# Kernel tuning notes

Measured on AMD Instinct MI355X. Metric: run time of the kernel, lower is better.

The kernel has to match this reference:

```python
import jax, jax.numpy as jnp
import numpy as np

K = 3  # kernel_size


def _build_grid(offset, H, W):
    """Vectorized version of the original double for-loop grid build.

    Original: for x in range(W), y in range(H):
        anchor = ([x, y] - [W-1, H-1]/2) / ([W-1, H-1]/2)
        fgrid[:, K*y:K*y+K, K*x:K*x+K, :] = offset[:, :, x, y].view(B, K, K, 2) + anchor
    Note offset is indexed [:, :, x, y] (x over range(W) on the H axis) -- requires H == W.
    """
    B = offset.shape[0]
    assert H == W, "original indexing offset[:, :, x, y] assumes square maps"
    o = offset.reshape(B, K, K, 2, H, W)          # [B, j, i, c, x-axis, y-axis]
    # -> [B, y, j, x, i, c] so rows are K*y+j, cols are K*x+i
    o = jnp.transpose(o, (0, 5, 1, 4, 2, 3))
    half_w = (W - 1) / 2.0
    half_h = (H - 1) / 2.0
    ax = ((jnp.arange(W, dtype=offset.dtype) - half_w) / half_w)  # anchor x-coord, indexed by x
    ay = ((jnp.arange(H, dtype=offset.dtype) - half_h) / half_h)  # anchor y-coord, indexed by y
    anch = jnp.stack(jnp.broadcast_arrays(ax[None, :], ay[:, None]), axis=-1)  # [H(y), W(x), 2]
    grid = o + anch[None, :, None, :, None, :]
    return grid.reshape(B, H * K, W * K, 2)


def _grid_sample_bilinear(img, grid):
    """F.grid_sample(img, grid, mode='bilinear', padding_mode='zeros', align_corners=False)."""
    B, C, H, W = img.shape
    gx, gy = grid[..., 0], grid[..., 1]          # [B, Ho, Wo]
    ix = ((gx + 1.0) * W - 1.0) * 0.5            # unnormalize, align_corners=False
    iy = ((gy + 1.0) * H - 1.0) * 0.5
    ix0 = jnp.floor(ix)
    iy0 = jnp.floor(iy)
    wx1 = ix - ix0
    wy1 = iy - iy0
    flat = img.reshape(B, C, H * W)

    def gather(xi, yi):
        valid = ((xi >= 0) & (xi <= W - 1) & (yi >= 0) & (yi <= H - 1))
        xc = jnp.clip(xi, 0, W - 1).astype(jnp.int32)
        yc = jnp.clip(yi, 0, H - 1).astype(jnp.int32)
        lin = (yc * W + xc).reshape(B, -1)       # [B, Ho*Wo]
        g = jax.vmap(lambda f, l: f[:, l])(flat, lin)  # [B, C, Ho*Wo]
        g = g.reshape(B, C, *xi.shape[1:])
        return g * valid[:, None].astype(img.dtype)

    out = (gather(ix0, iy0) * ((1 - wx1) * (1 - wy1))[:, None]
           + gather(ix0 + 1, iy0) * (wx1 * (1 - wy1))[:, None]
           + gather(ix0, iy0 + 1) * ((1 - wx1) * wy1)[:, None]
           + gather(ix0 + 1, iy0 + 1) * (wx1 * wy1)[:, None])
    return out


def setup_inputs() -> dict:
    key = jax.random.key(0)
    k1, k2, k3 = jax.random.split(key, 3)
    B, C, H, W = 32, 128, 56, 56
    OUTC = 256
    feature = jax.random.normal(k1, (B, C, H, W), dtype=jnp.float32)
    offset = jax.random.normal(k2, (B, 2 * K * K, H, W), dtype=jnp.float32) * 0.1
    conv_weight = jax.random.normal(k3, (OUTC, C, K, K), dtype=jnp.float32) * 0.05
    return {"feature": feature, "offset": offset, "conv_weight": conv_weight}


def reference(feature, offset, conv_weight):
    B, C, H, W = feature.shape
    grid = _build_grid(offset, H, W)                      # [B, H*K, W*K, 2]
    deformed = _grid_sample_bilinear(feature, grid)       # [B, C, H*K, W*K]
    out = jax.lax.conv_general_dilated(
        deformed, conv_weight, window_strides=(K, K), padding="VALID",
        dimension_numbers=("NCHW", "OIHW", "NCHW"))      # [B, OUTC, H, W]
    return out
```

## Files before the change

kernel.cpp:

```cpp
#include <hip/hip_runtime.h>
#include <hip/hip_bf16.h>
#include <stdint.h>

#define KTAPS 9
#define C_IN 128
#define C_OUT 256
#define HW 56
#define PLANE 3136
#define BATCH 32
#define NPX (BATCH * PLANE)
#define KTOT 1152
#define NBLK64 (NPX / 64)
#define BPER (NBLK64 / 8)
#define VBLK_STRIDE (KTAPS * 16384)

typedef __attribute__((ext_vector_type(8))) _Float16 f16x8;
typedef __attribute__((ext_vector_type(2))) _Float16 f16x2;
typedef __attribute__((ext_vector_type(4))) float f32x4;
typedef __attribute__((ext_vector_type(4))) unsigned int u32x4;

static __device__ __forceinline__ uint16_t f2h(float f) {
    _Float16 h = (_Float16)f;
    uint16_t u;
    __builtin_memcpy(&u, &h, 2);
    return u;
}

__global__ void k_feat_nhwc(const float* __restrict__ f, unsigned short* __restrict__ fws) {
    __shared__ float tile[C_IN * 57];
    int blk = blockIdx.x;
    int b = blk / HW, y = blk % HW;
    const float* src = f + (size_t)b * C_IN * PLANE + y * HW;
    for (int i = threadIdx.x; i < C_IN * HW; i += 256) {
        int c = i / HW, x = i % HW;
        tile[c * 57 + x] = src[(size_t)c * PLANE + x];
    }
    __syncthreads();
    unsigned short* dst = fws + (size_t)blk * HW * C_IN;
    for (int j = threadIdx.x; j < HW * C_IN; j += 256) {
        int x = j >> 7, c = j & 127;
        dst[j] = f2h(tile[c * 57 + x]);
    }
}

__global__ void k_weight(const float* __restrict__ w, unsigned short* __restrict__ W3) {
    int idx = blockIdx.x * 256 + threadIdx.x;
    if (idx >= C_OUT * KTOT) return;
    int e = idx & 7;
    int lane = (idx >> 3) & 63;
    int mtg = (idx >> 9) & 15;
    int ks = (idx >> 13) & 3;
    int t = idx >> 15;
    int oc = mtg * 16 + (lane & 15);
    int ic = ks * 32 + (lane >> 4) * 8 + e;
    int j = t / 3, i = t % 3;
    W3[idx] = f2h(w[((oc * C_IN + ic) * 3 + j) * 3 + i]);
}

__global__ void k_coords(const float* __restrict__ off, float* __restrict__ sxy) {
    __shared__ float tile[HW * 57];
    int blk = blockIdx.x;
    int b = blk / 18, tc = blk % 18;
    const float* src = off + (size_t)blk * PLANE;
    for (int i = threadIdx.x; i < PLANE; i += 256) {
        int xx = i / HW, yy = i % HW;
        tile[xx * 57 + yy] = src[i];
    }
    __syncthreads();
    float* dst = sxy + (size_t)tc * NPX + (size_t)b * PLANE;
    bool isx = (tc & 1) == 0;
    for (int p = threadIdx.x; p < PLANE; p += 256) {
        int y = p / HW, x = p % HW;
        float v = tile[x * 57 + y];
        float a = isx ? ((float)x - 27.5f) * (1.0f / 27.5f)
                      : ((float)y - 27.5f) * (1.0f / 27.5f);
        dst[p] = (v + a + 1.0f) * 28.0f - 0.5f;
    }
}

__global__ __launch_bounds__(256, 8) void k_sample(const unsigned short* __restrict__ fws,
                                                   const float* __restrict__ sxy,
                                                   unsigned char* __restrict__ V4) {
    __shared__ float cs[18][64];
    const int tid = threadIdx.x;
    const int wave = tid >> 6, lane = tid & 63;
    const int lb = (blockIdx.x & 7) * BPER + (blockIdx.x >> 3);
    const int gpx0 = lb * 64;
    for (int i = tid; i < 18 * 64; i += 256) {
        int tc = i >> 6, pp = i & 63;
        cs[tc][pp] = sxy[(size_t)tc * NPX + gpx0 + pp];
    }
    __syncthreads();

    const unsigned char* fimg =
        (const unsigned char*)(fws + (size_t)(gpx0 / PLANE) * (PLANE * C_IN));
    unsigned char* vblk = V4 + (size_t)lb * VBLK_STRIDE;
    const int q = lane >> 2, c = lane & 3;
    const int cx = c & 1, cy = c >> 1;
    const int pl = wave * 16 + q;
    const int lane4 = lane * 4;

    uint32_t d[4][4];
    f16x2 wv[4][4];

#pragma unroll
    for (int t = 0; t < KTAPS; t++) {
        float ixv = cs[2 * t][pl], iyv = cs[2 * t + 1][pl];
        float fx0 = floorf(ixv), fy0 = floorf(iyv);
        float wx1 = ixv - fx0, wy1 = iyv - fy0;
        int ix0 = (int)fx0, iy0 = (int)fy0;
        int xi = ix0 + cx, yi = iy0 + cy;
        float wf = (cx ? wx1 : 1.0f - wx1) * (cy ? wy1 : 1.0f - wy1);
        if ((unsigned)xi >= HW || (unsigned)yi >= HW) wf = 0.0f;
        int xc = min(max(xi, 0), HW - 1), yc = min(max(yi, 0), HW - 1);
        int offv = (yc * HW + xc) << 8;
        _Float16 hw_ = (_Float16)wf;
        uint16_t hu;
        __builtin_memcpy(&hu, &hw_, 2);
        int wpk = (int)((uint32_t)hu | ((uint32_t)hu << 16));

        auto ISS = [&](int qq, int slot) {
#pragma unroll
            for (int cc = 0; cc < 4; cc++) {
                int so_ = __builtin_amdgcn_readlane(offv, qq * 4 + cc);
                int wp_ = __builtin_amdgcn_readlane(wpk, qq * 4 + cc);
                __builtin_memcpy(&wv[slot][cc], &wp_, 4);
                d[slot][cc] = *(const uint32_t*)(fimg + so_ + lane4);
            }
        };
        auto FIN = [&](int qq, int slot) {
            f16x2 a0, a1, a2, a3;
            __builtin_memcpy(&a0, &d[slot][0], 4);
            __builtin_memcpy(&a1, &d[slot][1], 4);
            __builtin_memcpy(&a2, &d[slot][2], 4);
            __builtin_memcpy(&a3, &d[slot][3], 4);
            f16x2 v = a0 * wv[slot][0] + a1 * wv[slot][1] + a2 * wv[slot][2] + a3 * wv[slot][3];
            uint32_t u;
            __builtin_memcpy(&u, &v, 4);
            *(uint32_t*)(vblk + (size_t)t * 16384 + (wave * 16 + qq) * 256 + lane4) = u;
        };
        ISS(0, 0); ISS(1, 1); ISS(2, 2); ISS(3, 3);
#pragma unroll
        for (int qq = 0; qq < 16; qq++) {
            FIN(qq, qq & 3);
            if (qq < 12) ISS(qq + 4, (qq + 4) & 3);
        }
    }
}

__global__ __launch_bounds__(256, 3) void k_gemm(const unsigned short* __restrict__ W3,
                                                 const unsigned char* __restrict__ V4,
                                                 float* __restrict__ out) {
    __shared__ __align__(16) unsigned char Vt[2][16384];
    const int tid = threadIdx.x;
    const int wave = tid >> 6, lane = tid & 63;
    const int l16 = lane & 15, grp = lane >> 4;
    const int lb = (blockIdx.x & 7) * BPER + (blockIdx.x >> 3);
    const int gpx0 = lb * 64;
    const unsigned char* vblk = V4 + (size_t)lb * VBLK_STRIDE;

    f32x4 acc[4][4];
#pragma unroll
    for (int m = 0; m < 4; m++)
#pragma unroll
        for (int n = 0; n < 4; n++) acc[m][n] = (f32x4)0.0f;

    f16x8 A[2][4];
    u32x4 sv[4];

    auto SLOAD = [&](int t) {
#pragma unroll
        for (int j = 0; j < 4; j++)
            sv[j] = *(const u32x4*)(vblk + (size_t)t * 16384 + wave * 4096 + j * 1024 + lane * 16);
    };
    auto SWRITE = [&](int buf) {
#pragma unroll
        for (int j = 0; j < 4; j++) {
            int px = wave * 16 + j * 4 + (lane >> 4);
            int c16 = lane & 15;
            *(u32x4*)(&Vt[buf][px * 256 + ((c16 ^ (px & 7)) << 4)]) = sv[j];
        }
    };
    auto loadA = [&](int slot, int t, int ks) {
        const unsigned short* wb = W3 + (size_t)((t * 4 + ks) * 16 + wave * 4) * 512 + lane * 8;
#pragma unroll
        for (int mt = 0; mt < 4; mt++)
            A[slot][mt] = *(const f16x8*)(wb + mt * 512);
    };
    auto gemm_ks = [&](int ks, int buf, int slot) {
        f16x8 bv[4];
#pragma unroll
        for (int nt = 0; nt < 4; nt++) {
            int px = nt * 16 + l16;
            int g16 = ks * 4 + grp;
            bv[nt] = *(const f16x8*)(&Vt[buf][px * 256 + ((g16 ^ (px & 7)) << 4)]);
        }
#pragma unroll
        for (int mt = 0; mt < 4; mt++)
#pragma unroll
            for (int nt = 0; nt < 4; nt++)
                acc[mt][nt] = __builtin_amdgcn_mfma_f32_16x16x32_f16(A[slot][mt], bv[nt], acc[mt][nt], 0, 0, 0);
    };

    SLOAD(0);
    SWRITE(0);
    loadA(0, 0, 0);
    __syncthreads();

#pragma unroll
    for (int t = 0; t < KTAPS; t++) {
        const int buf = t & 1;
        const bool more = (t < KTAPS - 1);
        if (more) SLOAD(t + 1);
        loadA(1, t, 1);
        gemm_ks(0, buf, 0);
        loadA(0, t, 2);
        gemm_ks(1, buf, 1);
        loadA(1, t, 3);
        gemm_ks(2, buf, 0);
        if (more) loadA(0, t + 1, 0);
        gemm_ks(3, buf, 1);
        if (more) {
            __builtin_amdgcn_sched_barrier(0);
            SWRITE(buf ^ 1);
            __syncthreads();
        }
    }

    int bb = gpx0 / PLANE, rr0 = gpx0 - bb * PLANE;
    float* obase = out + (size_t)bb * C_OUT * PLANE + rr0 + l16;
#pragma unroll
    for (int nt = 0; nt < 4; nt++) {
        float* ob = obase + nt * 16;
#pragma unroll
        for (int mt = 0; mt < 4; mt++) {
#pragma unroll
            for (int r = 0; r < 4; r++) {
                int oc = wave * 64 + mt * 16 + grp * 4 + r;
                ob[(size_t)oc * PLANE] = acc[mt][nt][r];
            }
        }
    }
}

__global__ __launch_bounds__(256, 2) void k_fused(const unsigned short* __restrict__ fws,
                                                  const unsigned short* __restrict__ W3,
                                                  const float* __restrict__ sxy,
                                                  float* __restrict__ out) {
    __shared__ float cs[18][64];
    const int tid = threadIdx.x;
    const int wave = tid >> 6, lane = tid & 63;
    const int l16 = lane & 15, grp = lane >> 4;
    const int lbid = (blockIdx.x & 7) * (NBLK64 / 8) + (blockIdx.x >> 3);
    const int px0 = lbid * 64;
    const unsigned short* fb = fws + (size_t)(px0 / PLANE) * (PLANE * C_IN) + grp * 8;
    for (int i = tid; i < 18 * 64; i += 256) {
        int tc = i >> 6, pp = i & 63;
        cs[tc][pp] = sxy[(size_t)tc * NPX + px0 + pp];
    }
    __syncthreads();
    const int p = wave * 16 + l16;
    f32x4 acc[16];
#pragma unroll
    for (int m = 0; m < 16; m++) acc[m] = (f32x4)0.0f;
    f16x8 cv[4][4];
    float swc[4], swn[4];
    const unsigned short *c00, *c10, *c01, *c11;
    auto calc_tap = [&](int t, float* sw) {
        float ixv = cs[2 * t][p], iyv = cs[2 * t + 1][p];
        float fx0 = floorf(ixv), fy0 = floorf(iyv);
        float wx1 = ixv - fx0, wy1 = iyv - fy0;
        float wx0 = 1.0f - wx1, wy0 = 1.0f - wy1;
        int ix0 = (int)fx0, iy0 = (int)fy0, ix1 = ix0 + 1, iy1 = iy0 + 1;
        float vx0 = ((unsigned)ix0 < HW) ? 1.0f : 0.0f;
        float vx1 = ((unsigned)ix1 < HW) ? 1.0f : 0.0f;
        float vy0 = ((unsigned)iy0 < HW) ? 1.0f : 0.0f;
        float vy1 = ((unsigned)iy1 < HW) ? 1.0f : 0.0f;
        int xc0 = min(max(ix0, 0), HW - 1), xc1 = min(max(ix1, 0), HW - 1);
        int yc0 = min(max(iy0, 0), HW - 1), yc1 = min(max(iy1, 0), HW - 1);
        const unsigned short* r0 = fb + (size_t)(yc0 * HW) * C_IN;
        const unsigned short* r1 = fb + (size_t)(yc1 * HW) * C_IN;
        c00 = r0 + xc0 * C_IN; c10 = r0 + xc1 * C_IN;
        c01 = r1 + xc0 * C_IN; c11 = r1 + xc1 * C_IN;
        sw[0] = wx0 * wy0 * vx0 * vy0; sw[1] = wx1 * wy0 * vx1 * vy0;
        sw[2] = wx0 * wy1 * vx0 * vy1; sw[3] = wx1 * wy1 * vx1 * vy1;
    };
    auto sample_ks = [&](int ks) {
        cv[0][ks] = *(const f16x8*)(c00 + ks * 32);
        cv[1][ks] = *(const f16x8*)(c10 + ks * 32);
        cv[2][ks] = *(const f16x8*)(c01 + ks * 32);
        cv[3][ks] = *(const f16x8*)(c11 + ks * 32);
    };
    calc_tap(0, swc);
#pragma unroll
    for (int ks = 0; ks < 4; ks++) sample_ks(ks);
#pragma unroll
    for (int t = 0; t < KTAPS; t++) {
        const bool more = (t < KTAPS - 1);
        if (more) calc_tap(t + 1, swn);
#pragma unroll
        for (int ks = 0; ks < 4; ks++) {
            f16x8 v = cv[0][ks] * (f16x8)(_Float16)swc[0]
                    + cv[1][ks] * (f16x8)(_Float16)swc[1]
                    + cv[2][ks] * (f16x8)(_Float16)swc[2]
                    + cv[3][ks] * (f16x8)(_Float16)swc[3];
            const unsigned short* wb = W3 + (size_t)(t * 4 + ks) * 8192 + lane * 8;
            f16x8 af[16];
#pragma unroll
            for (int mtg = 0; mtg < 16; mtg++)
                af[mtg] = *(const f16x8*)(wb + mtg * 512);
            if (more) sample_ks(ks);
#pragma unroll
            for (int mtg = 0; mtg < 16; mtg++)
                acc[mtg] = __builtin_amdgcn_mfma_f32_16x16x32_f16(af[mtg], v, acc[mtg], 0, 0, 0);
        }
        if (more) {
#pragma unroll
            for (int c = 0; c < 4; c++) swc[c] = swn[c];
        }
    }
    int bb = px0 / PLANE, rr = px0 - bb * PLANE + p;
    float* ob = out + (size_t)bb * C_OUT * PLANE + rr;
#pragma unroll
    for (int mtg = 0; mtg < 16; mtg++)
#pragma unroll
        for (int r = 0; r < 4; r++)
            ob[(size_t)(mtg * 16 + grp * 4 + r) * PLANE] = acc[mtg][r];
}

extern "C" void kernel_launch(void* const* d_in, const int* in_sizes, int n_in,
                              void* d_out, int out_size, void* d_ws, size_t ws_size,
                              hipStream_t stream) {
    const float* feature = (const float*)d_in[0];
    const float* offset = (const float*)d_in[1];
    const float* weight = (const float*)d_in[2];
    float* out = (float*)d_out;

    char* ws = (char*)d_ws;
    unsigned short* fws = (unsigned short*)ws;
    unsigned short* W3 = (unsigned short*)(ws + 25690112);
    float* sxy = (float*)(ws + 25690112 + 589824);
    const size_t base = 25690112 + 589824 + 7225344;
    const size_t v4_full = (size_t)NBLK64 * VBLK_STRIDE;
    unsigned char* V4 = (unsigned char*)(ws + base);

    k_feat_nhwc<<<BATCH * HW, 256, 0, stream>>>(feature, fws);
    k_weight<<<(C_OUT * KTOT + 255) / 256, 256, 0, stream>>>(weight, W3);
    k_coords<<<BATCH * 18, 256, 0, stream>>>(offset, sxy);

    if (ws_size >= base + v4_full) {
        k_sample<<<NBLK64, 256, 0, stream>>>(fws, sxy, V4);
        k_gemm<<<NBLK64, 256, 0, stream>>>(W3, V4, out);
    } else {
        k_fused<<<NBLK64, 256, 0, stream>>>(fws, W3, sxy, out);
    }
}
```

Before: 226.7 us.

## Split sample/GEMM into two chunks and deepen GEMM prefetch pipeline

The sample and GEMM kernels now run in two half-size chunks that reuse a half-sized intermediate buffer. The aim is to keep the sampled fp16 tile buffer small enough to stay resident in the last-level cache between the producer and consumer kernels. The GEMM loop also prefetches global V data two taps ahead, loads all four K-slices of weights at once, and lowers launch bounds to 2 waves per SIMD. In exchange there are two extra kernel launches, higher register pressure and possibly lower occupancy.

```diff
diff --git a/kernel.cpp b/kernel.cpp
--- a/kernel.cpp
+++ b/kernel.cpp
@@ -11,7 +11,8 @@
 #define NPX (BATCH * PLANE)
 #define KTOT 1152
 #define NBLK64 (NPX / 64)
-#define BPER (NBLK64 / 8)
+#define CHBLK (NBLK64 / 2)
+#define CHPER (CHBLK / 8)
 #define VBLK_STRIDE (KTAPS * 16384)
 
 typedef __attribute__((ext_vector_type(8))) _Float16 f16x8;
@@ -80,12 +81,13 @@
 
 __global__ __launch_bounds__(256, 8) void k_sample(const unsigned short* __restrict__ fws,
                                                    const float* __restrict__ sxy,
-                                                   unsigned char* __restrict__ V4) {
+                                                   unsigned char* __restrict__ V4,
+                                                   int lb0) {
     __shared__ float cs[18][64];
     const int tid = threadIdx.x;
     const int wave = tid >> 6, lane = tid & 63;
-    const int lb = (blockIdx.x & 7) * BPER + (blockIdx.x >> 3);
-    const int gpx0 = lb * 64;
+    const int lb = (blockIdx.x & 7) * CHPER + (blockIdx.x >> 3);
+    const int gpx0 = (lb0 + lb) * 64;
     for (int i = tid; i < 18 * 64; i += 256) {
         int tc = i >> 6, pp = i & 63;
         cs[tc][pp] = sxy[(size_t)tc * NPX + gpx0 + pp];
@@ -148,15 +150,16 @@
     }
 }
 
-__global__ __launch_bounds__(256, 3) void k_gemm(const unsigned short* __restrict__ W3,
+__global__ __launch_bounds__(256, 2) void k_gemm(const unsigned short* __restrict__ W3,
                                                  const unsigned char* __restrict__ V4,
-                                                 float* __restrict__ out) {
+                                                 float* __restrict__ out,
+                                                 int lb0) {
     __shared__ __align__(16) unsigned char Vt[2][16384];
     const int tid = threadIdx.x;
     const int wave = tid >> 6, lane = tid & 63;
     const int l16 = lane & 15, grp = lane >> 4;
-    const int lb = (blockIdx.x & 7) * BPER + (blockIdx.x >> 3);
-    const int gpx0 = lb * 64;
+    const int lb = (blockIdx.x & 7) * CHPER + (blockIdx.x >> 3);
+    const int gpx0 = (lb0 + lb) * 64;
     const unsigned char* vblk = V4 + (size_t)lb * VBLK_STRIDE;
 
     f32x4 acc[4][4];
@@ -165,29 +168,29 @@
 #pragma unroll
         for (int n = 0; n < 4; n++) acc[m][n] = (f32x4)0.0f;
 
-    f16x8 A[2][4];
-    u32x4 sv[4];
-
-    auto SLOAD = [&](int t) {
+    f16x8 A[4][4];
+    u32x4 sv[2][4];
+
+    auto SLOAD = [&](int set, int t) {
 #pragma unroll
         for (int j = 0; j < 4; j++)
-            sv[j] = *(const u32x4*)(vblk + (size_t)t * 16384 + wave * 4096 + j * 1024 + lane * 16);
-    };
-    auto SWRITE = [&](int buf) {
+            sv[set][j] = *(const u32x4*)(vblk + (size_t)t * 16384 + wave * 4096 + j * 1024 + lane * 16);
+    };
+    auto SWRITE = [&](int set, int buf) {
 #pragma unroll
         for (int j = 0; j < 4; j++) {
             int px = wave * 16 + j * 4 + (lane >> 4);
             int c16 = lane & 15;
-            *(u32x4*)(&Vt[buf][px * 256 + ((c16 ^ (px & 7)) << 4)]) = sv[j];
-        }
-    };
-    auto loadA = [&](int slot, int t, int ks) {
+            *(u32x4*)(&Vt[buf][px * 256 + ((c16 ^ (px & 7)) << 4)]) = sv[set][j];
+        }
+    };
+    auto loadA = [&](int ks, int t) {
         const unsigned short* wb = W3 + (size_t)((t * 4 + ks) * 16 + wave * 4) * 512 + lane * 8;
 #pragma unroll
         for (int mt = 0; mt < 4; mt++)
-            A[slot][mt] = *(const f16x8*)(wb + mt * 512);
-    };
-    auto gemm_ks = [&](int ks, int buf, int slot) {
+            A[ks][mt] = *(const f16x8*)(wb + mt * 512);
+    };
+    auto gemm_ks = [&](int ks, int buf) {
         f16x8 bv[4];
 #pragma unroll
         for (int nt = 0; nt < 4; nt++) {
@@ -199,32 +202,24 @@
         for (int mt = 0; mt < 4; mt++)
 #pragma unroll
             for (int nt = 0; nt < 4; nt++)
-                acc[mt][nt] = __builtin_amdgcn_mfma_f32_16x16x32_f16(A[slot][mt], bv[nt], acc[mt][nt], 0, 0, 0);
-    };
-
-    SLOAD(0);
-    SWRITE(0);
-    loadA(0, 0, 0);
+                acc[mt][nt] = __builtin_amdgcn_mfma_f32_16x16x32_f16(A[ks][mt], bv[nt], acc[mt][nt], 0, 0, 0);
+    };
+
+    SLOAD(0, 0);
+    SWRITE(0, 0);
+    SLOAD(1, 1);
     __syncthreads();
 
 #pragma unroll
     for (int t = 0; t < KTAPS; t++) {
         const int buf = t & 1;
-        const bool more = (t < KTAPS - 1);
-        if (more) SLOAD(t + 1);
-        loadA(1, t, 1);
-        gemm_ks(0, buf, 0);
-        loadA(0, t, 2);
-        gemm_ks(1, buf, 1);
-        loadA(1, t, 3);
-        gemm_ks(2, buf, 0);
-        if (more) loadA(0, t + 1, 0);
-        gemm_ks(3, buf, 1);
-        if (more) {
-            __builtin_amdgcn_sched_barrier(0);
-            SWRITE(buf ^ 1);
-            __syncthreads();
-        }
+        if (t < KTAPS - 1) SWRITE((t + 1) & 1, (t + 1) & 1);
+        loadA(0, t); loadA(1, t); loadA(2, t); loadA(3, t);
+        __builtin_amdgcn_sched_barrier(0);
+        if (t < KTAPS - 2) SLOAD(t & 1, t + 2);
+        __builtin_amdgcn_sched_barrier(0);
+        gemm_ks(0, buf); gemm_ks(1, buf); gemm_ks(2, buf); gemm_ks(3, buf);
+        if (t < KTAPS - 1) __syncthreads();
     }
 
     int bb = gpx0 / PLANE, rr0 = gpx0 - bb * PLANE;
@@ -341,16 +336,18 @@
     unsigned short* W3 = (unsigned short*)(ws + 25690112);
     float* sxy = (float*)(ws + 25690112 + 589824);
     const size_t base = 25690112 + 589824 + 7225344;
-    const size_t v4_full = (size_t)NBLK64 * VBLK_STRIDE;
+    const size_t v4_half = (size_t)CHBLK * VBLK_STRIDE;
     unsigned char* V4 = (unsigned char*)(ws + base);
 
     k_feat_nhwc<<<BATCH * HW, 256, 0, stream>>>(feature, fws);
     k_weight<<<(C_OUT * KTOT + 255) / 256, 256, 0, stream>>>(weight, W3);
     k_coords<<<BATCH * 18, 256, 0, stream>>>(offset, sxy);
 
-    if (ws_size >= base + v4_full) {
-        k_sample<<<NBLK64, 256, 0, stream>>>(fws, sxy, V4);
-        k_gemm<<<NBLK64, 256, 0, stream>>>(W3, V4, out);
+    if (ws_size >= base + v4_half) {
+        for (int c = 0; c < 2; c++) {
+            k_sample<<<CHBLK, 256, 0, stream>>>(fws, sxy, V4, c * CHBLK);
+            k_gemm<<<CHBLK, 256, 0, stream>>>(W3, V4, out, c * CHBLK);
+        }
     } else {
         k_fused<<<NBLK64, 256, 0, stream>>>(fws, W3, sxy, out);
     }
```

Measured after the change: 203.2 us. -10.4%, faster.
